# Optimization experiments

Measured on AMD Instinct MI355X. Metric: run time of the kernel, lower is better.

The kernel has to match this reference:

```python
import jax, jax.numpy as jnp
import numpy as np

N, E = 50000, 800000
IN, HID, OUT = 256, 128, 64


def setup_inputs() -> dict:
    key = jax.random.key(0)
    ks = jax.random.split(key, 8)
    x = jax.random.normal(ks[0], (N, IN), dtype=jnp.float32)
    edge_index = jax.random.randint(ks[1], (2, E), 0, N, dtype=jnp.int64)
    # PyG GCNConv: Linear weight [out, in] (glorot-ish), bias [out] (zeros init; use small randn for a nontrivial baseline)
    W1 = jax.random.normal(ks[2], (HID, IN), dtype=jnp.float32) / np.sqrt(IN)
    b1 = jax.random.normal(ks[3], (HID,), dtype=jnp.float32) * 0.01
    Wmu = jax.random.normal(ks[4], (OUT, HID), dtype=jnp.float32) / np.sqrt(HID)
    bmu = jax.random.normal(ks[5], (OUT,), dtype=jnp.float32) * 0.01
    Wlv = jax.random.normal(ks[6], (OUT, HID), dtype=jnp.float32) / np.sqrt(HID)
    blv = jax.random.normal(ks[7], (OUT,), dtype=jnp.float32) * 0.01
    return {"x": x, "edge_index": edge_index, "W1": W1, "b1": b1,
            "Wmu": Wmu, "bmu": bmu, "Wlv": Wlv, "blv": blv}


def reference(x, edge_index, W1, b1, Wmu, bmu, Wlv, blv):
    n = x.shape[0]
    loop = jnp.arange(n, dtype=edge_index.dtype)
    src = jnp.concatenate([edge_index[0], loop])  # [E+N]
    dst = jnp.concatenate([edge_index[1], loop])
    # symmetric normalization with self-loops: deg computed on destinations
    deg = jax.ops.segment_sum(jnp.ones_like(dst, dtype=x.dtype), dst, num_segments=n)
    dis = jax.lax.rsqrt(deg)  # deg >= 1 due to self-loops
    norm = dis[src] * dis[dst]  # [E+N]

    def gcn(h, W, b):
        hw = h @ W.T                                   # [N, out]
        msg = hw[src] * norm[:, None]                  # [E+N, out] gather + scale
        return jax.ops.segment_sum(msg, dst, num_segments=n) + b

    h = jax.nn.relu(gcn(x, W1, b1))
    # dropout(p=0.5) is identity in eval mode
    return (gcn(h, Wmu, bmu), gcn(h, Wlv, blv))
```

## Files before the change

kernel.cpp:

```cpp
#include <hip/hip_runtime.h>

#define N_NODES 50000
#define N_EDGES 800000
#define DIN 256
#define DHID 128
#define DOUT 64
#define NB_SCAN 49
#define SENT N_NODES

typedef __attribute__((ext_vector_type(8))) short short8;
typedef __attribute__((ext_vector_type(4))) float f32x4;

static __device__ __forceinline__ short f2bf(float f) {
    union { float f; unsigned u; } v; v.f = f;
    unsigned r = v.u + 0x7FFFu + ((v.u >> 16) & 1u);
    return (short)(r >> 16);
}
static __device__ __forceinline__ float bflo(unsigned p) {
    union { unsigned u; float f; } v; v.u = p << 16; return v.f;
}
static __device__ __forceinline__ float bfhi(unsigned p) {
    union { unsigned u; float f; } v; v.u = p & 0xFFFF0000u; return v.f;
}


__global__ void count_kernel(const int* __restrict__ ei, int* __restrict__ cnt,
                             int* __restrict__ loc) {
    int stride = gridDim.x * blockDim.x;
    for (int e = blockIdx.x * blockDim.x + threadIdx.x; e < N_EDGES; e += stride) {
        loc[e] = atomicAdd(&cnt[ei[N_EDGES + e]], 1);
    }
}

__global__ __launch_bounds__(1024) void bsum_kernel(const int* __restrict__ cnt,
                                                    int* __restrict__ bsum) {
    __shared__ int ws[16];
    int tid = threadIdx.x, i = blockIdx.x * 1024 + tid;
    int v = (i < N_NODES) ? cnt[i] : 0;
    v = (v + 7) & ~7;
    #pragma unroll
    for (int off = 32; off >= 1; off >>= 1) v += __shfl_xor(v, off);
    if ((tid & 63) == 0) ws[tid >> 6] = v;
    __syncthreads();
    if (tid == 0) {
        int s = 0;
        #pragma unroll
        for (int w = 0; w < 16; ++w) s += ws[w];
        bsum[blockIdx.x] = s;
    }
}

__global__ void bscan_kernel(const int* __restrict__ bsum, int* __restrict__ bo,
                             int* __restrict__ rowptr) {
    int l = threadIdx.x;
    int v = (l < NB_SCAN) ? bsum[l] : 0;
    int x = v;
    #pragma unroll
    for (int off = 1; off < 64; off <<= 1) {
        int y = __shfl_up(x, off);
        if (l >= off) x += y;
    }
    if (l < NB_SCAN) bo[l] = x - v;
    if (l == 63) rowptr[N_NODES] = x;
}

__global__ __launch_bounds__(1024) void scan_apply_kernel(const int* __restrict__ cnt,
        const int* __restrict__ bo, int* __restrict__ rowptr,
        float* __restrict__ dis, int* __restrict__ col) {
    __shared__ int wsum[16];
    int tid = threadIdx.x, i = blockIdx.x * 1024 + tid;
    int lane = tid & 63, wid = tid >> 6;
    int v = (i < N_NODES) ? cnt[i] : 0;
    int p = (v + 7) & ~7;
    int x = p;
    #pragma unroll
    for (int off = 1; off < 64; off <<= 1) {
        int y = __shfl_up(x, off);
        if (lane >= off) x += y;
    }
    if (lane == 63) wsum[wid] = x;
    __syncthreads();
    if (tid == 0) {
        int s = 0;
        #pragma unroll
        for (int w = 0; w < 16; ++w) { int t = wsum[w]; wsum[w] = s; s += t; }
    }
    __syncthreads();
    int excl = bo[blockIdx.x] + wsum[wid] + (x - p);
    if (i < N_NODES) {
        rowptr[i] = excl;
        dis[i] = rsqrtf((float)(v + 1));
        for (int q = v; q < p; ++q) col[excl + q] = SENT;
    }
}

__global__ void fill_kernel(const int* __restrict__ ei, const int* __restrict__ loc,
                            const int* __restrict__ rowptr, int* __restrict__ col) {
    int stride = gridDim.x * blockDim.x;
    for (int e = blockIdx.x * blockDim.x + threadIdx.x; e < N_EDGES; e += stride) {
        int s = ei[e];
        int d = ei[N_EDGES + e];
        col[rowptr[d] + loc[e]] = s;
    }
}


__global__ void wprep_kernel(const float* __restrict__ W1, const float* __restrict__ Wmu,
                             const float* __restrict__ Wlv, short* __restrict__ W1b,
                             short* __restrict__ Wctb) {
    int tid = blockIdx.x * blockDim.x + threadIdx.x;
    if (tid < DHID * DIN) {
        W1b[tid] = f2bf(W1[tid]);
    } else if (tid < DHID * DIN + 2 * DOUT * DHID) {
        int t = tid - DHID * DIN;
        Wctb[t] = f2bf((t < DOUT * DHID) ? Wmu[t] : Wlv[t - DOUT * DHID]);
    }
}


__global__ __launch_bounds__(256) void xprep_kernel(const float* __restrict__ x,
        const float* __restrict__ dis, short* __restrict__ xb) {
    const int total = N_NODES * (DIN / 8);
    int stride = gridDim.x * blockDim.x;
    for (int c = blockIdx.x * blockDim.x + threadIdx.x; c < total; c += stride) {
        int row = c >> 5;
        float d = dis[row];
        const float* src = x + (size_t)c * 8;
        float4 f0 = *(const float4*)src;
        float4 f1 = *(const float4*)(src + 4);
        short8 o;
        o[0] = f2bf(f0.x * d); o[1] = f2bf(f0.y * d);
        o[2] = f2bf(f0.z * d); o[3] = f2bf(f0.w * d);
        o[4] = f2bf(f1.x * d); o[5] = f2bf(f1.y * d);
        o[6] = f2bf(f1.z * d); o[7] = f2bf(f1.w * d);
        *(short8*)(xb + (size_t)c * 8) = o;
    }
}


__global__ __launch_bounds__(256) void gemm1_mfma_kernel(const short* __restrict__ xb,
        const short* __restrict__ W1b, short* __restrict__ u1b) {
    const int lane = threadIdx.x & 63, w = threadIdx.x >> 6;
    const int l15 = lane & 15, kg = lane >> 4;
    const int rowg = w >> 1, colh = w & 1;
    const int nb = blockIdx.x * 32 + rowg * 16;
    const int r0 = nb + l15;
    const bool valid = r0 < N_NODES;
    const short* arow = xb + (size_t)r0 * DIN;

    f32x4 acc[4] = {};
    #pragma unroll
    for (int ks = 0; ks < 8; ++ks) {
        const int k0 = ks * 32 + kg * 8;
        short8 a = valid ? *(const short8*)(arow + k0)
                         : short8{0, 0, 0, 0, 0, 0, 0, 0};
        #pragma unroll
        for (int c = 0; c < 4; ++c) {
            const int cc = colh * 4 + c;
            short8 b = *(const short8*)(W1b + (size_t)(cc * 16 + l15) * DIN + k0);
            acc[c] = __builtin_amdgcn_mfma_f32_16x16x32_bf16(a, b, acc[c], 0, 0, 0);
        }
    }

    const int rb = nb + kg * 4;
    #pragma unroll
    for (int c = 0; c < 4; ++c) {
        const int j = (colh * 4 + c) * 16 + l15;
        #pragma unroll
        for (int e = 0; e < 4; ++e) {
            int r = rb + e;
            if (r < N_NODES)
                u1b[(size_t)r * DHID + j] = f2bf(acc[c][e]);
        }
    }
}


template <bool LAYER1>
__global__ __launch_bounds__(256) void pull_kernel(const int* __restrict__ rowptr,
        const int* __restrict__ col, const short* __restrict__ uin,
        const float* __restrict__ dis, const float* __restrict__ b1,
        unsigned* __restrict__ uout) {
    const int wid = threadIdx.x >> 6, lane = threadIdx.x & 63;
    const int i = blockIdx.x * 4 + wid;
    if (i >= N_NODES) return;
    const int beg = rowptr[i], end = rowptr[i + 1];
    const unsigned* __restrict__ up = (const unsigned*)uin;
    float ax = 0.f, ay = 0.f;
    for (int base = beg; base < end; base += 64) {
        const int rem = end - base;
        const int m = rem < 64 ? rem : 64;
        int cv = (lane < m) ? col[base + lane] : SENT;
        for (int t = 0; t < m; t += 8) {
            int c0 = __shfl(cv, t);
            int c1 = __shfl(cv, t + 1);
            int c2 = __shfl(cv, t + 2);
            int c3 = __shfl(cv, t + 3);
            int c4 = __shfl(cv, t + 4);
            int c5 = __shfl(cv, t + 5);
            int c6 = __shfl(cv, t + 6);
            int c7 = __shfl(cv, t + 7);
            unsigned v0 = up[(size_t)c0 * 64 + lane];
            unsigned v1 = up[(size_t)c1 * 64 + lane];
            unsigned v2 = up[(size_t)c2 * 64 + lane];
            unsigned v3 = up[(size_t)c3 * 64 + lane];
            unsigned v4 = up[(size_t)c4 * 64 + lane];
            unsigned v5 = up[(size_t)c5 * 64 + lane];
            unsigned v6 = up[(size_t)c6 * 64 + lane];
            unsigned v7 = up[(size_t)c7 * 64 + lane];
            ax += bflo(v0); ay += bfhi(v0);
            ax += bflo(v1); ay += bfhi(v1);
            ax += bflo(v2); ay += bfhi(v2);
            ax += bflo(v3); ay += bfhi(v3);
            ax += bflo(v4); ay += bfhi(v4);
            ax += bflo(v5); ay += bfhi(v5);
            ax += bflo(v6); ay += bfhi(v6);
            ax += bflo(v7); ay += bfhi(v7);
        }
    }
    const float di = dis[i];
    const unsigned sv = up[(size_t)i * 64 + lane];
    float tx = di * (ax + bflo(sv));
    float ty = di * (ay + bfhi(sv));
    if (LAYER1) {
        float2 b = *(const float2*)(b1 + lane * 2);
        tx = fmaxf(tx + b.x, 0.f) * di;
        ty = fmaxf(ty + b.y, 0.f) * di;
    }
    unsigned o = ((unsigned)(unsigned short)f2bf(tx)) |
                 (((unsigned)(unsigned short)f2bf(ty)) << 16);
    uout[(size_t)i * 64 + lane] = o;
}


__global__ __launch_bounds__(256) void gemm2_mfma_kernel(const short* __restrict__ a2b,
        const short* __restrict__ Wctb, const float* __restrict__ bmu,
        const float* __restrict__ blv, float* __restrict__ out) {
    const int lane = threadIdx.x & 63, w = threadIdx.x >> 6;
    const int l15 = lane & 15, kg = lane >> 4;
    const int nb = blockIdx.x * 64;
    const int r0 = nb + w * 16 + l15;
    const bool valid = r0 < N_NODES;
    const short* arow = a2b + (size_t)r0 * DHID;

    f32x4 acc[8] = {};
    #pragma unroll
    for (int ks = 0; ks < 4; ++ks) {
        const int k0 = ks * 32 + kg * 8;
        short8 a = valid ? *(const short8*)(arow + k0)
                         : short8{0, 0, 0, 0, 0, 0, 0, 0};
        #pragma unroll
        for (int c = 0; c < 8; ++c) {
            short8 b = *(const short8*)(Wctb + (size_t)(c * 16 + l15) * DHID + k0);
            acc[c] = __builtin_amdgcn_mfma_f32_16x16x32_bf16(a, b, acc[c], 0, 0, 0);
        }
    }

    float bias[8];
    #pragma unroll
    for (int c = 0; c < 8; ++c) {
        int j = c * 16 + l15;
        bias[c] = (j < DOUT) ? bmu[j] : blv[j - DOUT];
    }
    const int rb = nb + w * 16 + kg * 4;
    #pragma unroll
    for (int c = 0; c < 8; ++c) {
        const int j = c * 16 + l15;
        float* dst = (j < DOUT) ? (out + j)
                                : (out + (size_t)N_NODES * DOUT + (j - DOUT));
        #pragma unroll
        for (int e = 0; e < 4; ++e) {
            int r = rb + e;
            if (r < N_NODES)
                dst[(size_t)r * DOUT] = acc[c][e] + bias[c];
        }
    }
}


extern "C" void kernel_launch(void* const* d_in, const int* in_sizes, int n_in,
                              void* d_out, int out_size, void* d_ws, size_t ws_size,
                              hipStream_t stream) {
    const float* x   = (const float*)d_in[0];
    const int*   ei  = (const int*)d_in[1];
    const float* W1  = (const float*)d_in[2];
    const float* b1  = (const float*)d_in[3];
    const float* Wmu = (const float*)d_in[4];
    const float* bmu = (const float*)d_in[5];
    const float* Wlv = (const float*)d_in[6];
    const float* blv = (const float*)d_in[7];
    float* out = (float*)d_out;

    char* ws = (char*)d_ws;
    size_t off = 0;
    auto alloc = [&](size_t bytes) -> char* {
        char* p = ws + off;
        off += (bytes + 255) & ~(size_t)255;
        return p;
    };
    const size_t COL_CAP = (size_t)N_EDGES + 8 * (size_t)N_NODES + 64;
    int*   cnt    = (int*)  alloc((size_t)N_NODES * 4);
    int*   rowptr = (int*)  alloc((size_t)(N_NODES + 1) * 4);
    float* dis    = (float*)alloc((size_t)N_NODES * 4);
    int*   loc    = (int*)  alloc((size_t)N_EDGES * 4);
    int*   col    = (int*)  alloc(COL_CAP * 4);
    int*   bsum   = (int*)  alloc((size_t)NB_SCAN * 4);
    int*   bo     = (int*)  alloc((size_t)NB_SCAN * 4);
    short* W1b    = (short*)alloc((size_t)DHID * DIN * 2);
    short* Wctb   = (short*)alloc((size_t)2 * DOUT * DHID * 2);
    short* xb     = (short*)alloc((size_t)N_NODES * DIN * 2);
    short* u1b    = (short*)alloc((size_t)(N_NODES + 1) * DHID * 2);
    short* u2b    = (short*)alloc((size_t)(N_NODES + 1) * DHID * 2);
    short* a2b    = u1b;

    hipMemsetAsync(cnt, 0, (size_t)N_NODES * 4, stream);
    hipMemsetAsync(u1b + (size_t)N_NODES * DHID, 0, DHID * 2, stream);
    hipMemsetAsync(u2b + (size_t)N_NODES * DHID, 0, DHID * 2, stream);
    wprep_kernel<<<192, 256, 0, stream>>>(W1, Wmu, Wlv, W1b, Wctb);
    count_kernel<<<1024, 256, 0, stream>>>(ei, cnt, loc);
    bsum_kernel<<<NB_SCAN, 1024, 0, stream>>>(cnt, bsum);
    bscan_kernel<<<1, 64, 0, stream>>>(bsum, bo, rowptr);
    scan_apply_kernel<<<NB_SCAN, 1024, 0, stream>>>(cnt, bo, rowptr, dis, col);
    fill_kernel<<<1024, 256, 0, stream>>>(ei, loc, rowptr, col);
    xprep_kernel<<<2048, 256, 0, stream>>>(x, dis, xb);
    gemm1_mfma_kernel<<<(N_NODES + 31) / 32, 256, 0, stream>>>(xb, W1b, u1b);
    pull_kernel<true><<<N_NODES / 4, 256, 0, stream>>>(rowptr, col, u1b, dis, b1,
                                                       (unsigned*)u2b);
    pull_kernel<false><<<N_NODES / 4, 256, 0, stream>>>(rowptr, col, u2b, dis, nullptr,
                                                        (unsigned*)a2b);
    gemm2_mfma_kernel<<<(N_NODES + 63) / 64, 256, 0, stream>>>(a2b, Wctb, bmu, blv, out);
}
```

Baseline: 284.0 us.

## Widen pull unroll to 16 with padding, retile GEMM1, fold sentinel memsets into wprep

Result: no change. 281.8 us (-0.8%).

```diff
diff --git a/kernel.cpp b/kernel.cpp
--- a/kernel.cpp
+++ b/kernel.cpp
@@ -37,7 +37,7 @@
     __shared__ int ws[16];
     int tid = threadIdx.x, i = blockIdx.x * 1024 + tid;
     int v = (i < N_NODES) ? cnt[i] : 0;
-    v = (v + 7) & ~7;
+    v = (v + 15) & ~15;
     #pragma unroll
     for (int off = 32; off >= 1; off >>= 1) v += __shfl_xor(v, off);
     if ((tid & 63) == 0) ws[tid >> 6] = v;
@@ -71,7 +71,7 @@
     int tid = threadIdx.x, i = blockIdx.x * 1024 + tid;
     int lane = tid & 63, wid = tid >> 6;
     int v = (i < N_NODES) ? cnt[i] : 0;
-    int p = (v + 7) & ~7;
+    int p = (v + 15) & ~15;
     int x = p;
     #pragma unroll
     for (int off = 1; off < 64; off <<= 1) {
@@ -107,13 +107,18 @@
 
 __global__ void wprep_kernel(const float* __restrict__ W1, const float* __restrict__ Wmu,
                              const float* __restrict__ Wlv, short* __restrict__ W1b,
-                             short* __restrict__ Wctb) {
+                             short* __restrict__ Wctb, short* __restrict__ u1b,
+                             short* __restrict__ u2b) {
     int tid = blockIdx.x * blockDim.x + threadIdx.x;
     if (tid < DHID * DIN) {
         W1b[tid] = f2bf(W1[tid]);
     } else if (tid < DHID * DIN + 2 * DOUT * DHID) {
         int t = tid - DHID * DIN;
         Wctb[t] = f2bf((t < DOUT * DHID) ? Wmu[t] : Wlv[t - DOUT * DHID]);
+    } else if (tid < DHID * DIN + 2 * DOUT * DHID + DHID) {
+        int t = tid - (DHID * DIN + 2 * DOUT * DHID);
+        u1b[(size_t)SENT * DHID + t] = 0;
+        u2b[(size_t)SENT * DHID + t] = 0;
     }
 }
 
@@ -142,30 +147,28 @@
         const short* __restrict__ W1b, short* __restrict__ u1b) {
     const int lane = threadIdx.x & 63, w = threadIdx.x >> 6;
     const int l15 = lane & 15, kg = lane >> 4;
-    const int rowg = w >> 1, colh = w & 1;
-    const int nb = blockIdx.x * 32 + rowg * 16;
-    const int r0 = nb + l15;
+    const int nb = blockIdx.x * 64;
+    const int r0 = nb + w * 16 + l15;
     const bool valid = r0 < N_NODES;
     const short* arow = xb + (size_t)r0 * DIN;
 
-    f32x4 acc[4] = {};
+    f32x4 acc[8] = {};
     #pragma unroll
     for (int ks = 0; ks < 8; ++ks) {
         const int k0 = ks * 32 + kg * 8;
         short8 a = valid ? *(const short8*)(arow + k0)
                          : short8{0, 0, 0, 0, 0, 0, 0, 0};
         #pragma unroll
-        for (int c = 0; c < 4; ++c) {
-            const int cc = colh * 4 + c;
-            short8 b = *(const short8*)(W1b + (size_t)(cc * 16 + l15) * DIN + k0);
+        for (int c = 0; c < 8; ++c) {
+            short8 b = *(const short8*)(W1b + (size_t)(c * 16 + l15) * DIN + k0);
             acc[c] = __builtin_amdgcn_mfma_f32_16x16x32_bf16(a, b, acc[c], 0, 0, 0);
         }
     }
 
-    const int rb = nb + kg * 4;
-    #pragma unroll
-    for (int c = 0; c < 4; ++c) {
-        const int j = (colh * 4 + c) * 16 + l15;
+    const int rb = nb + w * 16 + kg * 4;
+    #pragma unroll
+    for (int c = 0; c < 8; ++c) {
+        const int j = c * 16 + l15;
         #pragma unroll
         for (int e = 0; e < 4; ++e) {
             int r = rb + e;
@@ -191,7 +194,7 @@
         const int rem = end - base;
         const int m = rem < 64 ? rem : 64;
         int cv = (lane < m) ? col[base + lane] : SENT;
-        for (int t = 0; t < m; t += 8) {
+        for (int t = 0; t < m; t += 16) {
             int c0 = __shfl(cv, t);
             int c1 = __shfl(cv, t + 1);
             int c2 = __shfl(cv, t + 2);
@@ -200,6 +203,14 @@
             int c5 = __shfl(cv, t + 5);
             int c6 = __shfl(cv, t + 6);
             int c7 = __shfl(cv, t + 7);
+            int c8 = __shfl(cv, t + 8);
+            int c9 = __shfl(cv, t + 9);
+            int ca = __shfl(cv, t + 10);
+            int cb = __shfl(cv, t + 11);
+            int cc = __shfl(cv, t + 12);
+            int cd = __shfl(cv, t + 13);
+            int ce = __shfl(cv, t + 14);
+            int cf = __shfl(cv, t + 15);
             unsigned v0 = up[(size_t)c0 * 64 + lane];
             unsigned v1 = up[(size_t)c1 * 64 + lane];
             unsigned v2 = up[(size_t)c2 * 64 + lane];
@@ -208,6 +219,14 @@
             unsigned v5 = up[(size_t)c5 * 64 + lane];
             unsigned v6 = up[(size_t)c6 * 64 + lane];
             unsigned v7 = up[(size_t)c7 * 64 + lane];
+            unsigned v8 = up[(size_t)c8 * 64 + lane];
+            unsigned v9 = up[(size_t)c9 * 64 + lane];
+            unsigned va = up[(size_t)ca * 64 + lane];
+            unsigned vb = up[(size_t)cb * 64 + lane];
+            unsigned vc = up[(size_t)cc * 64 + lane];
+            unsigned vd = up[(size_t)cd * 64 + lane];
+            unsigned ve = up[(size_t)ce * 64 + lane];
+            unsigned vf = up[(size_t)cf * 64 + lane];
             ax += bflo(v0); ay += bfhi(v0);
             ax += bflo(v1); ay += bfhi(v1);
             ax += bflo(v2); ay += bfhi(v2);
@@ -216,6 +235,14 @@
             ax += bflo(v5); ay += bfhi(v5);
             ax += bflo(v6); ay += bfhi(v6);
             ax += bflo(v7); ay += bfhi(v7);
+            ax += bflo(v8); ay += bfhi(v8);
+            ax += bflo(v9); ay += bfhi(v9);
+            ax += bflo(va); ay += bfhi(va);
+            ax += bflo(vb); ay += bfhi(vb);
+            ax += bflo(vc); ay += bfhi(vc);
+            ax += bflo(vd); ay += bfhi(vd);
+            ax += bflo(ve); ay += bfhi(ve);
+            ax += bflo(vf); ay += bfhi(vf);
         }
     }
     const float di = dis[i];
@@ -298,7 +325,7 @@
         off += (bytes + 255) & ~(size_t)255;
         return p;
     };
-    const size_t COL_CAP = (size_t)N_EDGES + 8 * (size_t)N_NODES + 64;
+    const size_t COL_CAP = (size_t)N_EDGES + 16 * (size_t)N_NODES + 64;
     int*   cnt    = (int*)  alloc((size_t)N_NODES * 4);
     int*   rowptr = (int*)  alloc((size_t)(N_NODES + 1) * 4);
     float* dis    = (float*)alloc((size_t)N_NODES * 4);
@@ -314,16 +341,14 @@
     short* a2b    = u1b;
 
     hipMemsetAsync(cnt, 0, (size_t)N_NODES * 4, stream);
-    hipMemsetAsync(u1b + (size_t)N_NODES * DHID, 0, DHID * 2, stream);
-    hipMemsetAsync(u2b + (size_t)N_NODES * DHID, 0, DHID * 2, stream);
-    wprep_kernel<<<192, 256, 0, stream>>>(W1, Wmu, Wlv, W1b, Wctb);
+    wprep_kernel<<<193, 256, 0, stream>>>(W1, Wmu, Wlv, W1b, Wctb, u1b, u2b);
     count_kernel<<<1024, 256, 0, stream>>>(ei, cnt, loc);
     bsum_kernel<<<NB_SCAN, 1024, 0, stream>>>(cnt, bsum);
     bscan_kernel<<<1, 64, 0, stream>>>(bsum, bo, rowptr);
     scan_apply_kernel<<<NB_SCAN, 1024, 0, stream>>>(cnt, bo, rowptr, dis, col);
     fill_kernel<<<1024, 256, 0, stream>>>(ei, loc, rowptr, col);
     xprep_kernel<<<2048, 256, 0, stream>>>(x, dis, xb);
-    gemm1_mfma_kernel<<<(N_NODES + 31) / 32, 256, 0, stream>>>(xb, W1b, u1b);
+    gemm1_mfma_kernel<<<(N_NODES + 63) / 64, 256, 0, stream>>>(xb, W1b, u1b);
     pull_kernel<true><<<N_NODES / 4, 256, 0, stream>>>(rowptr, col, u1b, dis, b1,
                                                        (unsigned*)u2b);
     pull_kernel<false><<<N_NODES / 4, 256, 0, stream>>>(rowptr, col, u2b, dis, nullptr,
```
